# Kernel tuning notes

Hardware: AMD Instinct MI355X
Metric: run time of the kernel (lower is better)

The kernel has to match this reference:

```python
import jax, jax.numpy as jnp
import numpy as np

# Model constants (match init_kwargs)
L = 32              # one_side_length (effective_L)
ED = 32             # embed_dim = n_ssm (repeat = 1)
ND = 2              # ndim
DIR = 4             # directions_amount
KD = DIR * ED       # kernel_dim = 128
R = 2 * L ** 3      # coeff_matrix_row_amount = 65536
V = 2 * L           # power_dim = 64
SCALE = (1.0 / ND) ** 0.5
B_IMG, H_IMG = 8, 64


def setup_inputs() -> dict:
    key = jax.random.key(0)
    ks = jax.random.split(key, 24)
    inp = {}
    inp['x'] = jax.random.normal(ks[0], (B_IMG, H_IMG, H_IMG, ED), jnp.float32)
    i = 1
    for d in ('h', 'v'):
        for s in ('A1', 'A2', 'A3', 'A4'):
            inp[f'M{d}_{s}'] = jax.random.uniform(ks[i], (R, V), jnp.float32); i += 1
        inp[f'M{d}_B'] = jax.random.uniform(ks[i], (R, 2), jnp.float32); i += 1
    for p in ('A_1', 'A_2', 'A_3', 'A_4', 'B_1', 'B_2', 'C_1', 'C_2'):
        inp[p] = jax.random.normal(ks[i], (KD, ND), jnp.float32); i += 1
    inp['W'] = jax.random.normal(ks[i], (ED, ED), jnp.float32); i += 1
    inp['b'] = jnp.zeros((ED,), jnp.float32)
    return inp


def _compute_kernel(Ms_h, Ms_v, A_list, B_1, B_2, C_1, C_2):
    # A powers via exp/log trick: [V, KD, ND]
    ell = jnp.arange(V, dtype=jnp.float32)
    Apow = [jnp.exp(ell[:, None, None] * jnp.log(jax.nn.sigmoid(a))[None]) for a in A_list]
    Bstk = jnp.stack([jax.nn.sigmoid(B_1), jax.nn.sigmoid(B_2)], 0)  # [2, KD, ND]
    vecs = Apow + [Bstk]
    outs = []
    for Ms in (Ms_h, Ms_v):
        prod = None
        for M, vec in zip(Ms, vecs):
            cur = jnp.einsum('rv,vhn->rhn', M, vec)  # [R, KD, ND]
            prod = cur if prod is None else prod * cur
        # [L^2, R/L^2, KD, ND] -> sum over r2 -> [L^2, KD, ND]
        outs.append(prod.reshape(L * L, R // (L * L), KD, ND).sum(axis=1))
    out = (jnp.einsum('lhn,hn->lh', outs[0], C_1 * SCALE)
           + jnp.einsum('lhn,hn->lh', outs[1], C_2 * SCALE))
    out = out.reshape(L, L, KD)
    # boundary corrections (first row/col doubled, corner net-unchanged)
    out = out.at[0, :, :].multiply(2.0)
    out = out.at[:, 0, :].multiply(2.0)
    out = out.at[0, 0].divide(4.0)
    return out  # [L, L, KD]


def _forward(x, Ms_h, Ms_v, A_list, B_1, B_2, C_1, C_2, W, b):
    xc = jnp.transpose(x, (0, 3, 1, 2))  # b c h w  (transpose=True path)
    H = xc.shape[-1]
    k = jnp.transpose(_compute_kernel(Ms_h, Ms_v, A_list, B_1, B_2, C_1, C_2), (2, 0, 1))  # [KD, L, L]
    pad = H - L
    k = jnp.pad(k, ((0, 0), (0, pad), (0, pad)))  # [KD, H, H]
    s2 = (2 * H, 2 * H)
    flips = [(), (2,), (3,), (2, 3)]
    y = None
    for i, fl in enumerate(flips):
        ki = k[i * ED:(i + 1) * ED]  # [ED, H, H] (repeat == 1)
        xi = jnp.flip(xc, fl) if fl else xc
        xf = jnp.fft.rfft2(xi, s=s2)
        kf = jnp.fft.rfft2(ki, s=s2)
        cur = jnp.fft.irfft2(xf * kf, s=s2)[..., :H, :H]
        cur = jnp.flip(cur, fl) if fl else cur
        y = cur if y is None else y + cur
    y = jnp.transpose(y, (0, 2, 3, 1))  # b h w c
    return y @ W.T + b  # mixing linear layer on channels


def reference(x, Mh_A1, Mh_A2, Mh_A3, Mh_A4, Mh_B,
              Mv_A1, Mv_A2, Mv_A3, Mv_A4, Mv_B,
              A_1, A_2, A_3, A_4, B_1, B_2, C_1, C_2, W, b):
    Ms_h = (Mh_A1, Mh_A2, Mh_A3, Mh_A4, Mh_B)
    Ms_v = (Mv_A1, Mv_A2, Mv_A3, Mv_A4, Mv_B)
    return _forward(x, Ms_h, Ms_v, [A_1, A_2, A_3, A_4], B_1, B_2, C_1, C_2, W, b)
```

## Files before the change

### kernel.cpp

```cpp
#include <hip/hip_runtime.h>
#include <hip/hip_fp16.h>

typedef _Float16 f16x8 __attribute__((ext_vector_type(8)));
typedef _Float16 half4v __attribute__((ext_vector_type(4)));
typedef float float4v __attribute__((ext_vector_type(4)));
typedef __attribute__((ext_vector_type(8))) short short8;
typedef __attribute__((ext_vector_type(16))) float f32x16;

#define WS_BFH   0
#define WS_BSG   65536
#define WS_OUTS  66048
#define WS_KC    590336
#define WS_XPAD  719360
#define WS_YC    1767936
#define WS_TF    2816512

__device__ inline unsigned short f2bf(float f) {
  unsigned int u = __float_as_uint(f);
  u += 0x7fffu + ((u >> 16) & 1u);
  return (unsigned short)(u >> 16);
}

__global__ void k0_prep(const float* __restrict__ A1, const float* __restrict__ A2,
                        const float* __restrict__ A3, const float* __restrict__ A4,
                        const float* __restrict__ B1, const float* __restrict__ B2,
                        _Float16* __restrict__ Bfh, float* __restrict__ bsg) {
  const int blk = blockIdx.x;
  const int i = blk >> 1, kb = blk & 1;
  const int hn = threadIdx.x;
  const float* As[4] = {A1, A2, A3, A4};
  const float a = As[i][hn];
  const float s = 1.0f / (1.0f + expf(-a));
  float p = 1.0f;
  for (int v = 0; v < kb * 32; ++v) p *= s;
  const int ntile = hn >> 4;
  #pragma unroll
  for (int g = 0; g < 4; ++g) {
    _Float16 h[8];
    #pragma unroll
    for (int j = 0; j < 8; ++j) { h[j] = (_Float16)p; p *= s; }
    const int lane = (hn & 15) | (g << 4);
    _Float16* dst = Bfh + ((((i * 2 + kb) * 16 + ntile) * 64 + lane) << 3);
    *(f16x8*)dst = *(f16x8*)h;
  }
  if (blk == 0) {
    bsg[hn]       = 1.0f / (1.0f + expf(-B1[hn]));
    bsg[256 + hn] = 1.0f / (1.0f + expf(-B2[hn]));
  }
}

__global__ __launch_bounds__(256, 4) void k1_mfma(
    const float* __restrict__ Mh0, const float* __restrict__ Mh1,
    const float* __restrict__ Mh2, const float* __restrict__ Mh3,
    const float* __restrict__ MhB,
    const float* __restrict__ Mv0, const float* __restrict__ Mv1,
    const float* __restrict__ Mv2, const float* __restrict__ Mv3,
    const float* __restrict__ MvB,
    const _Float16* __restrict__ Bfh, const float* __restrict__ bsg,
    float* __restrict__ outs) {
  __shared__ _Float16 Alds[4 * 4 * 2 * 64 * 8];
  __shared__ float MBs[128];
  __shared__ float bsgs[512];

  const int bd = blockIdx.x >> 10;
  const int l  = blockIdx.x & 1023;
  const float* Ms[4] = {bd ? Mv0 : Mh0, bd ? Mv1 : Mh1, bd ? Mv2 : Mh2, bd ? Mv3 : Mh3};
  const float* MB    = bd ? MvB : MhB;
  const int t = threadIdx.x;

  if (t < 128) MBs[t] = MB[l * 128 + t];
  bsgs[t]       = bsg[t];
  bsgs[256 + t] = bsg[256 + t];

  #pragma unroll
  for (int i = 0; i < 4; ++i) {
    const float* M = Ms[i] + l * 4096;
    #pragma unroll
    for (int c0 = 0; c0 < 4; ++c0) {
      const int c = t + c0 * 256;
      const int row = c >> 4;
      const int v4  = (c & 15) << 2;
      const float4 f = *(const float4*)(M + row * 64 + v4);
      const int m     = row >> 4;
      const int lane2 = (row & 15) | (((v4 >> 3) & 3) << 4);
      const int kb    = v4 >> 5;
      const int jj    = v4 & 7;
      half4v* dst = (half4v*)&Alds[((((i * 4 + m) * 2 + kb) * 64 + lane2) << 3) + jj];
      *dst = (half4v){(_Float16)f.x, (_Float16)f.y, (_Float16)f.z, (_Float16)f.w};
    }
  }
  __syncthreads();

  const int w    = t >> 6;
  const int lane = t & 63;
  const int q = lane >> 4, col = lane & 15;

  #pragma unroll
  for (int half = 0; half < 2; ++half) {
    float4v E[4][2];
    #pragma unroll
    for (int i = 0; i < 4; ++i) {
      float4v acc[4][2];
      #pragma unroll
      for (int m = 0; m < 4; ++m)
        #pragma unroll
        for (int n = 0; n < 2; ++n) acc[m][n] = (float4v){0.f, 0.f, 0.f, 0.f};
      f16x8 Bf[2][2];
      #pragma unroll
      for (int kb = 0; kb < 2; ++kb)
        #pragma unroll
        for (int n = 0; n < 2; ++n)
          Bf[kb][n] = *(const f16x8*)(Bfh +
              ((((i * 2 + kb) * 16 + (w * 4 + half * 2 + n)) * 64 + lane) << 3));
      #pragma unroll
      for (int kb = 0; kb < 2; ++kb)
        #pragma unroll
        for (int m = 0; m < 4; ++m) {
          const f16x8 Af = *(const f16x8*)&Alds[((((i * 4 + m) * 2 + kb) * 64 + lane) << 3)];
          #pragma unroll
          for (int n = 0; n < 2; ++n)
            acc[m][n] = __builtin_amdgcn_mfma_f32_16x16x32_f16(Af, Bf[kb][n], acc[m][n], 0, 0, 0);
        }
      if (i == 0) {
        #pragma unroll
        for (int m = 0; m < 4; ++m)
          #pragma unroll
          for (int n = 0; n < 2; ++n) E[m][n] = acc[m][n];
      } else {
        #pragma unroll
        for (int m = 0; m < 4; ++m)
          #pragma unroll
          for (int n = 0; n < 2; ++n) E[m][n] *= acc[m][n];
      }
    }

    #pragma unroll
    for (int n = 0; n < 2; ++n) {
      const int hn = w * 64 + (half * 2 + n) * 16 + col;
      const float b0 = bsgs[hn], b1 = bsgs[256 + hn];
      float ssum = 0.f;
      #pragma unroll
      for (int m = 0; m < 4; ++m)
        #pragma unroll
        for (int r = 0; r < 4; ++r) {
          const int row = m * 16 + q * 4 + r;
          const float bdot = MBs[row * 2] * b0 + MBs[row * 2 + 1] * b1;
          ssum = fmaf(E[m][n][r], bdot, ssum);
        }
      ssum += __shfl_xor(ssum, 16);
      ssum += __shfl_xor(ssum, 32);
      if (lane < 16) outs[(bd * 1024 + l) * 256 + hn] = ssum;
    }
  }
}

__global__ void k2_kc(const float* __restrict__ outs, const float* __restrict__ C1,
                      const float* __restrict__ C2, float* __restrict__ kc) {
  const int c = blockIdx.x;
  const float SC = 0.70710678118654752f;
  for (int idx = threadIdx.x; idx < 63 * 64; idx += 256) {
    const int U = idx >> 6, V = idx & 63;
    float acc = 0.f;
    if (V < 63) {
      const int u = U - 31, v = V - 31;
      #pragma unroll
      for (int d = 0; d < 4; ++d) {
        const int dy = (d == 1 || d == 3) ? u : -u;
        const int dx = (d == 2 || d == 3) ? v : -v;
        if (dy >= 0 && dy < 32 && dx >= 0 && dx < 32) {
          const int l = dy * 32 + dx;
          const int h = d * 32 + c;
          const float e = (dy == 0 && dx == 0) ? 1.f : ((dy == 0 || dx == 0) ? 2.f : 1.f);
          const float s0 = outs[l * 256 + h * 2 + 0] * C1[h * 2 + 0]
                         + outs[l * 256 + h * 2 + 1] * C1[h * 2 + 1];
          const float s1 = outs[262144 + l * 256 + h * 2 + 0] * C2[h * 2 + 0]
                         + outs[262144 + l * 256 + h * 2 + 1] * C2[h * 2 + 1];
          acc += e * SC * (s0 + s1);
        }
      }
    }
    kc[(c * 63 + U) * 64 + V] = acc;
  }
}

__global__ void k2b_tfrag(const float* __restrict__ kc, unsigned short* __restrict__ Tf) {
  const int cu = blockIdx.x;
  const float* kcr = kc + cu * 64;
  const int t = threadIdx.x;
  #pragma unroll
  for (int s = 0; s < 2; ++s) {
    const int slot = t + s * 256;
    const int f = slot >> 6, lane = slot & 63;
    const int kt = f >> 1, nt = f & 1;
    const int kbase = kt * 16 + (lane >> 5) * 8;
    const int n = nt * 32 + (lane & 31);
    unsigned int o[4];
    #pragma unroll
    for (int jp = 0; jp < 4; ++jp) {
      unsigned short h0, h1;
      {
        const int v = (kbase + 2 * jp) - n + 31;
        h0 = (v >= 0 && v < 63) ? f2bf(kcr[v]) : 0;
      }
      {
        const int v = (kbase + 2 * jp + 1) - n + 31;
        h1 = (v >= 0 && v < 63) ? f2bf(kcr[v]) : 0;
      }
      o[jp] = (unsigned int)h0 | ((unsigned int)h1 << 16);
    }
    unsigned int* dst = (unsigned int*)(Tf + (cu * 8 + f) * 512 + lane * 8);
    dst[0] = o[0]; dst[1] = o[1]; dst[2] = o[2]; dst[3] = o[3];
  }
}

__global__ void k3_xt(const float* __restrict__ x, unsigned short* __restrict__ Xpad) {
  __shared__ float ls[4 * 64 * 33];
  const int b = blockIdx.x >> 4, pt = blockIdx.x & 15;
  const int t = threadIdx.x;
  const float* src = x + (b * 64 + pt * 4) * 2048;
  #pragma unroll 8
  for (int k = 0; k < 32; ++k) {
    const int e = t + k * 256;
    const int p = e >> 11, q = (e >> 5) & 63, cl = e & 31;
    ls[(p * 64 + q) * 33 + cl] = src[e];
  }
  unsigned int* Xp32 = (unsigned int*)Xpad;
  if (pt == 0) {
    for (int idx = t; idx < 31744; idx += 256) {
      const int c = idx / 992, r = idx - c * 992;
      Xp32[(b * 32 + c) * 4032 + r] = 0u;
    }
  }
  if (pt == 15) {
    for (int idx = t; idx < 31744; idx += 256) {
      const int c = idx / 992, r = idx - c * 992;
      Xp32[(b * 32 + c) * 4032 + 3040 + r] = 0u;
    }
  }
  __syncthreads();
  #pragma unroll 8
  for (int k = 0; k < 16; ++k) {
    const int o = t + k * 256;
    const int cl = o >> 7, p = (o >> 5) & 3, q2 = o & 31;
    const float f0 = ls[(p * 64 + 2 * q2 + 0) * 33 + cl];
    const float f1 = ls[(p * 64 + 2 * q2 + 1) * 33 + cl];
    const unsigned int pk = (unsigned int)f2bf(f0) | ((unsigned int)f2bf(f1) << 16);
    Xp32[(b * 32 + cl) * 4032 + (pt * 4 + p + 31) * 32 + q2] = pk;
  }
}

__global__ __launch_bounds__(256, 1) void k4b_conv(const unsigned short* __restrict__ Xpad,
                                                   const unsigned short* __restrict__ Tf,
                                                   float* __restrict__ yc) {
  __shared__ float red[4 * 4096];
  const int bc = blockIdx.x;
  const int c  = bc & 31;
  const int t = threadIdx.x, w = t >> 6, lane = t & 63;
  const unsigned short* Xp = Xpad + bc * 8064;
  const unsigned short* Tc = Tf + c * 63 * 4096;
  const int r = lane & 31, kh = lane >> 5;

  f32x16 acc[2][2];
  #pragma unroll
  for (int m = 0; m < 2; ++m)
    #pragma unroll
    for (int n = 0; n < 2; ++n)
      #pragma unroll
      for (int e = 0; e < 16; ++e) acc[m][n][e] = 0.f;

  short8 Ac[2][4], Bc[4][2];
  int u = w;
  #pragma unroll
  for (int m = 0; m < 2; ++m)
    #pragma unroll
    for (int kt = 0; kt < 4; ++kt)
      Ac[m][kt] = *(const short8*)(Xp + (m * 32 + r + u) * 64 + kt * 16 + kh * 8);
  #pragma unroll
  for (int kt = 0; kt < 4; ++kt)
    #pragma unroll
    for (int nt = 0; nt < 2; ++nt)
      Bc[kt][nt] = *(const short8*)(Tc + (u * 8 + kt * 2 + nt) * 512 + lane * 8);

  for (int i = 0; i < 16; ++i) {
    const int un = u + 4;
    const bool has_next = (un < 63);
    short8 An[2][4], Bn[4][2];
    if (has_next) {
      #pragma unroll
      for (int m = 0; m < 2; ++m)
        #pragma unroll
        for (int kt = 0; kt < 4; ++kt)
          An[m][kt] = *(const short8*)(Xp + (m * 32 + r + un) * 64 + kt * 16 + kh * 8);
      #pragma unroll
      for (int kt = 0; kt < 4; ++kt)
        #pragma unroll
        for (int nt = 0; nt < 2; ++nt)
          Bn[kt][nt] = *(const short8*)(Tc + (un * 8 + kt * 2 + nt) * 512 + lane * 8);
    }
    #pragma unroll
    for (int kt = 0; kt < 4; ++kt)
      #pragma unroll
      for (int m = 0; m < 2; ++m)
        #pragma unroll
        for (int nt = 0; nt < 2; ++nt)
          acc[m][nt] = __builtin_amdgcn_mfma_f32_32x32x16_bf16(Ac[m][kt], Bc[kt][nt],
                                                               acc[m][nt], 0, 0, 0);
    if (!has_next) break;
    #pragma unroll
    for (int m = 0; m < 2; ++m)
      #pragma unroll
      for (int kt = 0; kt < 4; ++kt) Ac[m][kt] = An[m][kt];
    #pragma unroll
    for (int kt = 0; kt < 4; ++kt)
      #pragma unroll
      for (int nt = 0; nt < 2; ++nt) Bc[kt][nt] = Bn[kt][nt];
    u = un;
  }

  float* my = red + w * 4096;
  #pragma unroll
  for (int m = 0; m < 2; ++m)
    #pragma unroll
    for (int nt = 0; nt < 2; ++nt)
      #pragma unroll
      for (int e = 0; e < 16; ++e) {
        const int row = (e & 3) + 8 * (e >> 2) + 4 * kh;
        my[(m * 32 + row) * 64 + nt * 32 + r] = acc[m][nt][e];
      }
  __syncthreads();
  float* out = yc + bc * 4096;
  #pragma unroll
  for (int k = 0; k < 16; ++k) {
    const int idx = t + k * 256;
    out[idx] = red[idx] + red[4096 + idx] + red[8192 + idx] + red[12288 + idx];
  }
}

__global__ void k5_out(const float* __restrict__ yc, const float* __restrict__ W,
                       const float* __restrict__ bias, float* __restrict__ out) {
  __shared__ float ysh[64 * 33];
  const int b = blockIdx.x >> 6, p = blockIdx.x & 63;
  const int t = threadIdx.x;
  const float* ybp = yc + b * 131072 + p * 64;
  #pragma unroll
  for (int k = 0; k < 8; ++k) {
    const int f = t + k * 256;
    const int cch = f >> 6, q = f & 63;
    ysh[q * 33 + cch] = ybp[cch * 4096 + q];
  }
  const int e = t & 31;
  float wr[32];
  #pragma unroll
  for (int c4 = 0; c4 < 8; ++c4) {
    const float4 f4 = *(const float4*)(W + e * 32 + c4 * 4);
    wr[c4 * 4 + 0] = f4.x; wr[c4 * 4 + 1] = f4.y;
    wr[c4 * 4 + 2] = f4.z; wr[c4 * 4 + 3] = f4.w;
  }
  const float bb = bias[e];
  __syncthreads();
  const int q0 = t >> 5;
  #pragma unroll
  for (int k = 0; k < 8; ++k) {
    const int q = q0 + k * 8;
    float a = bb;
    #pragma unroll
    for (int cc = 0; cc < 32; ++cc) a = fmaf(ysh[q * 33 + cc], wr[cc], a);
    out[((b * 64 + p) * 64 + q) * 32 + e] = a;
  }
}

extern "C" void kernel_launch(void* const* d_in, const int* in_sizes, int n_in,
                              void* d_out, int out_size, void* d_ws, size_t ws_size,
                              hipStream_t stream) {
  const float* x   = (const float*)d_in[0];
  const float* Mh[5] = {(const float*)d_in[1], (const float*)d_in[2], (const float*)d_in[3],
                        (const float*)d_in[4], (const float*)d_in[5]};
  const float* Mv[5] = {(const float*)d_in[6], (const float*)d_in[7], (const float*)d_in[8],
                        (const float*)d_in[9], (const float*)d_in[10]};
  const float* A1 = (const float*)d_in[11];
  const float* A2 = (const float*)d_in[12];
  const float* A3 = (const float*)d_in[13];
  const float* A4 = (const float*)d_in[14];
  const float* B1 = (const float*)d_in[15];
  const float* B2 = (const float*)d_in[16];
  const float* C1 = (const float*)d_in[17];
  const float* C2 = (const float*)d_in[18];
  const float* W  = (const float*)d_in[19];
  const float* bb = (const float*)d_in[20];
  float* ws  = (float*)d_ws;
  _Float16* Bfh = (_Float16*)(ws + WS_BFH);
  float* bsg  = ws + WS_BSG;
  float* outs = ws + WS_OUTS;
  float* kc   = ws + WS_KC;
  unsigned short* Xpad = (unsigned short*)(ws + WS_XPAD);
  float* yc   = ws + WS_YC;
  unsigned short* Tf = (unsigned short*)(ws + WS_TF);

  k0_prep<<<8, 256, 0, stream>>>(A1, A2, A3, A4, B1, B2, Bfh, bsg);
  k3_xt<<<128, 256, 0, stream>>>(x, Xpad);
  k1_mfma<<<2048, 256, 0, stream>>>(Mh[0], Mh[1], Mh[2], Mh[3], Mh[4],
                                    Mv[0], Mv[1], Mv[2], Mv[3], Mv[4],
                                    Bfh, bsg, outs);
  k2_kc<<<32, 256, 0, stream>>>(outs, C1, C2, kc);
  k2b_tfrag<<<2016, 256, 0, stream>>>(kc, Tf);
  k4b_conv<<<256, 256, 0, stream>>>(Xpad, Tf, yc);
  k5_out<<<512, 256, 0, stream>>>(yc, W, bb, (float*)d_out);
}
```

Before: 272.8 us.

## Make coefficient-matrix MFMA kernel persistent with double-buffered direct-to-LDS loads

k1_mfma changes from 2048 one-shot blocks to 256 persistent blocks that each process 8 row groups. Each block double-buffers fp32 M tiles in padded LDS, filled with global_load_lds so the next tile loads while the current one computes. The B fragments are loaded into registers once per block, and the fp16 conversion moves to LDS read time. k2_kc is also split across 256 blocks instead of 32 to add parallelism. The costs are higher register pressure (launch bounds lowered to 1 block per CU) and twice the LDS per block, since tiles are now stored as fp32.

Measured after the change: 277.0 us. About the same (+1.5%).

```diff
diff --git a/kernel.cpp b/kernel.cpp
--- a/kernel.cpp
+++ b/kernel.cpp
@@ -2,7 +2,6 @@
 #include <hip/hip_fp16.h>
 
 typedef _Float16 f16x8 __attribute__((ext_vector_type(8)));
-typedef _Float16 half4v __attribute__((ext_vector_type(4)));
 typedef float float4v __attribute__((ext_vector_type(4)));
 typedef __attribute__((ext_vector_type(8))) short short8;
 typedef __attribute__((ext_vector_type(16))) float f32x16;
@@ -15,10 +14,17 @@
 #define WS_YC    1767936
 #define WS_TF    2816512
 
+#define AROW 260
+
 __device__ inline unsigned short f2bf(float f) {
   unsigned int u = __float_as_uint(f);
   u += 0x7fffu + ((u >> 16) & 1u);
   return (unsigned short)(u >> 16);
+}
+
+__device__ __forceinline__ void gl_lds16(const void* g, void* l) {
+  __builtin_amdgcn_global_load_lds((const __attribute__((address_space(1))) void*)g,
+                                   (__attribute__((address_space(3))) void*)l, 16, 0, 0);
 }
 
 __global__ void k0_prep(const float* __restrict__ A1, const float* __restrict__ A2,
@@ -49,7 +55,7 @@
   }
 }
 
-__global__ __launch_bounds__(256, 4) void k1_mfma(
+__global__ __launch_bounds__(256, 1) void k1_mfma(
     const float* __restrict__ Mh0, const float* __restrict__ Mh1,
     const float* __restrict__ Mh2, const float* __restrict__ Mh3,
     const float* __restrict__ MhB,
@@ -58,95 +64,108 @@
     const float* __restrict__ MvB,
     const _Float16* __restrict__ Bfh, const float* __restrict__ bsg,
     float* __restrict__ outs) {
-  __shared__ _Float16 Alds[4 * 4 * 2 * 64 * 8];
-  __shared__ float MBs[128];
+  __shared__ __align__(16) float Abuf[2][64 * AROW + 128];
   __shared__ float bsgs[512];
 
-  const int bd = blockIdx.x >> 10;
-  const int l  = blockIdx.x & 1023;
-  const float* Ms[4] = {bd ? Mv0 : Mh0, bd ? Mv1 : Mh1, bd ? Mv2 : Mh2, bd ? Mv3 : Mh3};
-  const float* MB    = bd ? MvB : MhB;
   const int t = threadIdx.x;
-
-  if (t < 128) MBs[t] = MB[l * 128 + t];
+  const int w = t >> 6, lane = t & 63;
+  const int g = lane >> 4, cc = lane & 15;
+
   bsgs[t]       = bsg[t];
   bsgs[256 + t] = bsg[256 + t];
 
-  #pragma unroll
-  for (int i = 0; i < 4; ++i) {
-    const float* M = Ms[i] + l * 4096;
-    #pragma unroll
-    for (int c0 = 0; c0 < 4; ++c0) {
-      const int c = t + c0 * 256;
-      const int row = c >> 4;
-      const int v4  = (c & 15) << 2;
-      const float4 f = *(const float4*)(M + row * 64 + v4);
-      const int m     = row >> 4;
-      const int lane2 = (row & 15) | (((v4 >> 3) & 3) << 4);
-      const int kb    = v4 >> 5;
-      const int jj    = v4 & 7;
-      half4v* dst = (half4v*)&Alds[((((i * 4 + m) * 2 + kb) * 64 + lane2) << 3) + jj];
-      *dst = (half4v){(_Float16)f.x, (_Float16)f.y, (_Float16)f.z, (_Float16)f.w};
-    }
-  }
-  __syncthreads();
-
-  const int w    = t >> 6;
-  const int lane = t & 63;
-  const int q = lane >> 4, col = lane & 15;
-
-  #pragma unroll
-  for (int half = 0; half < 2; ++half) {
-    float4v E[4][2];
+  f16x8 Bf[4][2][4];
+  #pragma unroll
+  for (int i = 0; i < 4; ++i)
+    #pragma unroll
+    for (int kb = 0; kb < 2; ++kb)
+      #pragma unroll
+      for (int n = 0; n < 4; ++n)
+        Bf[i][kb][n] = *(const f16x8*)(Bfh +
+            ((((i * 2 + kb) * 16 + (w * 4 + n)) * 64 + lane) << 3));
+
+  auto stage = [&](int buf, int gi) {
+    const int bd = gi >> 10, l = gi & 1023;
+    const float* M0 = bd ? Mv0 : Mh0;
+    const float* M1 = bd ? Mv1 : Mh1;
+    const float* M2 = bd ? Mv2 : Mh2;
+    const float* M3 = bd ? Mv3 : Mh3;
+    const float* mp = (g == 0) ? M0 : (g == 1) ? M1 : (g == 2) ? M2 : M3;
+    const float* gp = mp + (size_t)(l * 64) * 64 + cc * 4;
+    float* lb = &Abuf[buf][0];
+    #pragma unroll
+    for (int it = 0; it < 16; ++it) {
+      const int r = w * 16 + it;
+      gl_lds16(gp + r * 64, lb + r * AROW);
+    }
+    if (w == 0 && lane < 32) {
+      const float* MBp = bd ? MvB : MhB;
+      gl_lds16(MBp + l * 128 + lane * 4, lb + 64 * AROW);
+    }
+  };
+
+  stage(0, blockIdx.x);
+
+  for (int k = 0; k < 8; ++k) {
+    __syncthreads();
+    if (k < 7) stage((k + 1) & 1, blockIdx.x + ((k + 1) << 8));
+
+    const int gi = blockIdx.x + (k << 8);
+    const int bd = gi >> 10, l = gi & 1023;
+    const float* Ap = &Abuf[k & 1][0];
+
+    float4v E[4][4];
     #pragma unroll
     for (int i = 0; i < 4; ++i) {
-      float4v acc[4][2];
+      float4v acc[4][4];
       #pragma unroll
       for (int m = 0; m < 4; ++m)
         #pragma unroll
-        for (int n = 0; n < 2; ++n) acc[m][n] = (float4v){0.f, 0.f, 0.f, 0.f};
-      f16x8 Bf[2][2];
+        for (int n = 0; n < 4; ++n) acc[m][n] = (float4v){0.f, 0.f, 0.f, 0.f};
       #pragma unroll
       for (int kb = 0; kb < 2; ++kb)
         #pragma unroll
-        for (int n = 0; n < 2; ++n)
-          Bf[kb][n] = *(const f16x8*)(Bfh +
-              ((((i * 2 + kb) * 16 + (w * 4 + half * 2 + n)) * 64 + lane) << 3));
-      #pragma unroll
-      for (int kb = 0; kb < 2; ++kb)
-        #pragma unroll
         for (int m = 0; m < 4; ++m) {
-          const f16x8 Af = *(const f16x8*)&Alds[((((i * 4 + m) * 2 + kb) * 64 + lane) << 3)];
+          const float* ar = Ap + (m * 16 + cc) * AROW + i * 64 + kb * 32 + g * 8;
+          const float4 f0 = *(const float4*)ar;
+          const float4 f1 = *(const float4*)(ar + 4);
+          const f16x8 Af = {(_Float16)f0.x, (_Float16)f0.y, (_Float16)f0.z, (_Float16)f0.w,
+                            (_Float16)f1.x, (_Float16)f1.y, (_Float16)f1.z, (_Float16)f1.w};
           #pragma unroll
-          for (int n = 0; n < 2; ++n)
-            acc[m][n] = __builtin_amdgcn_mfma_f32_16x16x32_f16(Af, Bf[kb][n], acc[m][n], 0, 0, 0);
+          for (int n = 0; n < 4; ++n)
+            acc[m][n] = __builtin_amdgcn_mfma_f32_16x16x32_f16(Af, Bf[i][kb][n], acc[m][n], 0, 0, 0);
         }
       if (i == 0) {
         #pragma unroll
         for (int m = 0; m < 4; ++m)
           #pragma unroll
-          for (int n = 0; n < 2; ++n) E[m][n] = acc[m][n];
+          for (int n = 0; n < 4; ++n) E[m][n] = acc[m][n];
       } else {
         #pragma unroll
         for (int m = 0; m < 4; ++m)
           #pragma unroll
-          for (int n = 0; n < 2; ++n) E[m][n] *= acc[m][n];
+          for (int n = 0; n < 4; ++n) E[m][n] *= acc[m][n];
       }
     }
 
-    #pragma unroll
-    for (int n = 0; n < 2; ++n) {
-      const int hn = w * 64 + (half * 2 + n) * 16 + col;
+    const float* MBl = Ap + 64 * AROW;
+    float2 mb[16];
+    #pragma unroll
+    for (int m = 0; m < 4; ++m)
+      #pragma unroll
+      for (int r = 0; r < 4; ++r)
+        mb[m * 4 + r] = *(const float2*)(MBl + (m * 16 + g * 4 + r) * 2);
+
+    #pragma unroll
+    for (int n = 0; n < 4; ++n) {
+      const int hn = w * 64 + n * 16 + cc;
       const float b0 = bsgs[hn], b1 = bsgs[256 + hn];
       float ssum = 0.f;
       #pragma unroll
       for (int m = 0; m < 4; ++m)
         #pragma unroll
-        for (int r = 0; r < 4; ++r) {
-          const int row = m * 16 + q * 4 + r;
-          const float bdot = MBs[row * 2] * b0 + MBs[row * 2 + 1] * b1;
-          ssum = fmaf(E[m][n][r], bdot, ssum);
-        }
+        for (int r = 0; r < 4; ++r)
+          ssum = fmaf(E[m][n][r], mb[m * 4 + r].x * b0 + mb[m * 4 + r].y * b1, ssum);
       ssum += __shfl_xor(ssum, 16);
       ssum += __shfl_xor(ssum, 32);
       if (lane < 16) outs[(bd * 1024 + l) * 256 + hn] = ssum;
@@ -156,9 +175,10 @@
 
 __global__ void k2_kc(const float* __restrict__ outs, const float* __restrict__ C1,
                       const float* __restrict__ C2, float* __restrict__ kc) {
-  const int c = blockIdx.x;
+  const int c = blockIdx.x >> 3;
+  const int base = (blockIdx.x & 7) * 504;
   const float SC = 0.70710678118654752f;
-  for (int idx = threadIdx.x; idx < 63 * 64; idx += 256) {
+  for (int idx = base + threadIdx.x; idx < base + 504 && idx < 63 * 64; idx += 256) {
     const int U = idx >> 6, V = idx & 63;
     float acc = 0.f;
     if (V < 63) {
@@ -398,10 +418,10 @@
 
   k0_prep<<<8, 256, 0, stream>>>(A1, A2, A3, A4, B1, B2, Bfh, bsg);
   k3_xt<<<128, 256, 0, stream>>>(x, Xpad);
-  k1_mfma<<<2048, 256, 0, stream>>>(Mh[0], Mh[1], Mh[2], Mh[3], Mh[4],
-                                    Mv[0], Mv[1], Mv[2], Mv[3], Mv[4],
-                                    Bfh, bsg, outs);
-  k2_kc<<<32, 256, 0, stream>>>(outs, C1, C2, kc);
+  k1_mfma<<<256, 256, 0, stream>>>(Mh[0], Mh[1], Mh[2], Mh[3], Mh[4],
+                                   Mv[0], Mv[1], Mv[2], Mv[3], Mv[4],
+                                   Bfh, bsg, outs);
+  k2_kc<<<256, 256, 0, stream>>>(outs, C1, C2, kc);
   k2b_tfrag<<<2016, 256, 0, stream>>>(kc, Tf);
   k4b_conv<<<256, 256, 0, stream>>>(Xpad, Tf, yc);
   k5_out<<<512, 256, 0, stream>>>(yc, W, bb, (float*)d_out);
```
